# Kernel optimization log

Measured on AMD Instinct MI355X. Metric: run time of the kernel, lower is better.

Reference implementation:

```python
import jax, jax.numpy as jnp
import numpy as np

N_NODES = 50000
N_EDGES = 800000
IN_C = 128
HID_C = 128
OUT_C = 128
ATT_H = 64
EPS_COS = 1e-8
EPS_EUD = 1e-6


def _cos_sim(a, b):
    # torch.cosine_similarity(dim=1): dot / max(|a|*|b|, eps)
    num = jnp.sum(a * b, axis=1)
    den = jnp.maximum(jnp.linalg.norm(a, axis=1) * jnp.linalg.norm(b, axis=1), EPS_COS)
    return num / den


def _eud(a, b):
    # nn.PairwiseDistance(p=2): ||a - b + eps||_2
    d = a - b + EPS_EUD
    return jnp.sqrt(jnp.sum(d * d, axis=1))


def _sage(x, row, col, ew, Wl, bl, Wr):
    # SAGEConv with edge weights: mean_j(ew_ij * x_j) @ Wl + bl + x_i @ Wr
    msg = x[col] * ew[:, None]                               # [E, C]
    agg = jax.ops.segment_sum(msg, row, num_segments=N_NODES)  # [N, C]
    deg = jax.ops.segment_sum(jnp.ones_like(ew), row, num_segments=N_NODES)
    agg = agg / jnp.maximum(deg, 1.0)[:, None]
    return agg @ Wl + bl + x @ Wr


def setup_inputs() -> dict:
    key = jax.random.key(0)
    ks = jax.random.split(key, 12)
    s = 0.05
    return {
        "x": jax.random.normal(ks[0], (N_NODES, IN_C), jnp.float32),
        "row": jax.random.randint(ks[1], (N_EDGES,), 0, N_NODES),
        "col": jax.random.randint(ks[2], (N_EDGES,), 0, N_NODES),
        "Wl0": jax.random.normal(ks[3], (IN_C, HID_C), jnp.float32) * s,
        "bl0": jax.random.normal(ks[4], (HID_C,), jnp.float32) * s,
        "Wr0": jax.random.normal(ks[5], (IN_C, HID_C), jnp.float32) * s,
        "Wl1": jax.random.normal(ks[6], (HID_C, OUT_C), jnp.float32) * s,
        "bl1": jax.random.normal(ks[7], (OUT_C,), jnp.float32) * s,
        "Wr1": jax.random.normal(ks[8], (HID_C, OUT_C), jnp.float32) * s,
        "attW1": jax.random.normal(ks[9], (HID_C, ATT_H), jnp.float32) * s,
        "attb1": jax.random.normal(ks[10], (ATT_H,), jnp.float32) * s,
        "attW2": jax.random.normal(ks[11], (ATT_H, 1), jnp.float32) * s,
    }


def reference(x, row, col, Wl0, bl0, Wr0, Wl1, bl1, Wr1, attW1, attb1, attW2):
    xs, xd = x[row], x[col]
    # cosine branch (dropout is a no-op in eval mode)
    e_cos = _cos_sim(xs, xd)
    x3 = jax.nn.relu(_sage(x, row, col, e_cos, Wl0, bl0, Wr0))   # [N, HID]
    e_cos2 = _cos_sim(x3[row], x3[col])
    x1 = _sage(x3, row, col, e_cos2, Wl1, bl1, Wr1)              # [N, OUT]
    # euclidean branch
    e_eud = _eud(xs, xd)
    x4 = jax.nn.relu(_sage(x, row, col, e_eud, Wl0, bl0, Wr0))   # [N, HID]
    e_eud2 = _eud(x4[row], x4[col])
    x2 = _sage(x4, row, col, e_eud2, Wl1, bl1, Wr1)              # [N, OUT]
    # attention pooling over the 4 branch embeddings
    z = jnp.stack([x1, x2, x3, x4], axis=1)                      # [N, 4, C]
    w = jnp.tanh(z @ attW1 + attb1) @ attW2                      # [N, 4, 1]
    beta = jax.nn.softmax(w, axis=1)
    emb = jnp.sum(beta * z, axis=1)                              # [N, C]
    return (emb, x3, x4)
```

## Files before the change

kernel.cpp:

```cpp
#include <hip/hip_runtime.h>

#define NN 50000
#define NE 800000
#define C 128
#define CAP 64
#define CAPSH 6

typedef __attribute__((ext_vector_type(8))) short short8_t;
typedef __attribute__((ext_vector_type(4))) float f32x4;
typedef __attribute__((ext_vector_type(2))) float f32x2;
typedef __attribute__((ext_vector_type(2))) _Float16 half2_t;
typedef __attribute__((ext_vector_type(8))) _Float16 half8_t;

__device__ __forceinline__ unsigned short f2h_u(float f) {
    _Float16 h = (_Float16)f;
    union { _Float16 h; unsigned short u; } v; v.h = h; return v.u;
}

__device__ __forceinline__ float fdot2(half2_t a, half2_t b, float c) {
#if __has_builtin(__builtin_amdgcn_fdot2)
    return __builtin_amdgcn_fdot2(a, b, c, false);
#else
    return c + (float)a.x * (float)b.x + (float)a.y * (float)b.y;
#endif
}

__device__ __forceinline__ float rsq_fast(float x) {
#if __has_builtin(__builtin_amdgcn_rsqf)
    return __builtin_amdgcn_rsqf(x);
#else
    float r; asm volatile("v_rsq_f32 %0, %1" : "=v"(r) : "v"(x)); return r;
#endif
}
__device__ __forceinline__ float sqrt_fast(float x) {
#if __has_builtin(__builtin_amdgcn_sqrtf)
    return __builtin_amdgcn_sqrtf(x);
#else
    float r; asm volatile("v_sqrt_f32 %0, %1" : "=v"(r) : "v"(x)); return r;
#endif
}

template <int CTRL>
__device__ __forceinline__ float dpp_add(float x) {
    int y = __builtin_amdgcn_update_dpp(0, __float_as_int(x), CTRL, 0xF, 0xF, false);
    return x + __int_as_float(y);
}
__device__ __forceinline__ float qred16(float x) {
    x = dpp_add<0xB1>(x);
    x = dpp_add<0x4E>(x);
    x = dpp_add<0x141>(x);
    x = dpp_add<0x140>(x);
    return x;
}

#define BUCK_NB ((NE / 4 + 255) / 256)
#define CAST_NB (NN / 4)
#define PREP_NB ((65536 + 8192) / 256)
__global__ void cast_prep(const float* __restrict__ x, unsigned short* __restrict__ xh,
                          float2* __restrict__ st1,
                          const float* __restrict__ Wl0, const float* __restrict__ Wr0,
                          const float* __restrict__ Wl1, const float* __restrict__ Wr1,
                          const float* __restrict__ aW1,
                          unsigned short* __restrict__ Bt, unsigned short* __restrict__ BtA,
                          const int* __restrict__ row, const int* __restrict__ col,
                          int* __restrict__ cnt, int* __restrict__ colv) {
    if (blockIdx.x < BUCK_NB) {
        int base = (blockIdx.x * 256 + threadIdx.x) * 4;
        if (base < NE) {
            int4 r4 = *(const int4*)(row + base);
            int4 c4 = *(const int4*)(col + base);
            int p0 = atomicAdd(&cnt[r4.x], 1);
            int p1 = atomicAdd(&cnt[r4.y], 1);
            int p2 = atomicAdd(&cnt[r4.z], 1);
            int p3 = atomicAdd(&cnt[r4.w], 1);
            if (p0 < CAP) colv[(r4.x << CAPSH) + p0] = c4.x;
            if (p1 < CAP) colv[(r4.y << CAPSH) + p1] = c4.y;
            if (p2 < CAP) colv[(r4.z << CAPSH) + p2] = c4.z;
            if (p3 < CAP) colv[(r4.w << CAPSH) + p3] = c4.w;
        }
    } else if (blockIdx.x < BUCK_NB + CAST_NB) {
        int node = (blockIdx.x - BUCK_NB) * 4 + (threadIdx.x >> 6);
        int lane = threadIdx.x & 63;
        float2 v = *(const float2*)(x + (size_t)node * C + lane * 2);
        half2_t h; h.x = (_Float16)v.x; h.y = (_Float16)v.y;
        *(half2_t*)(xh + (size_t)node * C + lane * 2) = h;
        float sq = v.x * v.x + v.y * v.y;
        float sm = v.x + v.y;
#pragma unroll
        for (int off = 32; off > 0; off >>= 1) {
            sq += __shfl_xor(sq, off, 64);
            sm += __shfl_xor(sm, off, 64);
        }
        if (lane == 0) st1[node] = make_float2(sq, sm);
    } else {
        int id = (blockIdx.x - BUCK_NB - CAST_NB) * 256 + threadIdx.x;
        if (id < 65536) {
            int layer = id >> 15;
            int c = (id >> 14) & 1;
            int n = (id >> 7) & 127;
            int kk = id & 127;
            const float* W = layer == 0 ? (c == 0 ? Wl0 : Wr0) : (c == 0 ? Wl1 : Wr1);
            Bt[id] = f2h_u(W[kk * 128 + n]);
        } else {
            int a = id - 65536;
            int cl = a >> 7, k = a & 127;
            BtA[a] = f2h_u(aW1[k * 64 + cl]);
        }
    }
}

__global__ __launch_bounds__(256) void fused_l1(
    const unsigned short* __restrict__ xh, const int* __restrict__ colv,
    const int* __restrict__ cnts, const float2* __restrict__ st1,
    unsigned short* __restrict__ aggc, unsigned short* __restrict__ agge) {
    int node = blockIdx.x * 4 + (threadIdx.x >> 6);
    int lane = threadIdx.x & 63;
    int q = lane >> 4, lq = lane & 15;
    int cnt_raw = cnts[node];
    int cnt = cnt_raw < CAP ? cnt_raw : CAP;
    int cv = colv[(node << CAPSH) + lane];
    half8_t xr = *(const half8_t*)(xh + (size_t)node * C + lq * 8);
    float2 sr = st1[node];
    float n2r = sr.x, s1r = sr.y;
    f32x2 ac[4] = {};
    f32x2 ae[4] = {};
    for (int p = 0; p < cnt; p += 4) {
        int ei = p + q;
        bool valid = ei < cnt;
        int src = valid ? ei : (cnt - 1);
        int c0 = __shfl(cv, src, 64);
        half8_t u = *(const half8_t*)(xh + (size_t)c0 * C + lq * 8);
        float2 t0 = st1[c0];
        float d = 0.f;
#pragma unroll
        for (int i = 0; i < 4; ++i) {
            half2_t a; a.x = xr[2 * i]; a.y = xr[2 * i + 1];
            half2_t b; b.x = u[2 * i]; b.y = u[2 * i + 1];
            d = fdot2(a, b, d);
        }
        d = qred16(d);
        float wc0 = d * rsq_fast(fmaxf(n2r * t0.x, 1e-16f));
        float qq = n2r + t0.x - 2.f * d + 2e-6f * (s1r - t0.y) + 1.28e-10f;
        float we0 = sqrt_fast(fmaxf(qq, 0.f));
        if (!valid) { wc0 = 0.f; we0 = 0.f; }
        f32x2 wcv; wcv.x = wc0; wcv.y = wc0;
        f32x2 wev; wev.x = we0; wev.y = we0;
#pragma unroll
        for (int i = 0; i < 4; ++i) {
            f32x2 uf; uf.x = (float)u[2 * i]; uf.y = (float)u[2 * i + 1];
            ac[i] += wcv * uf;
            ae[i] += wev * uf;
        }
    }
#pragma unroll
    for (int i = 0; i < 4; ++i) {
#pragma unroll
        for (int k = 0; k < 2; ++k) {
            float vc = ac[i][k], ve = ae[i][k];
            vc += __shfl_xor(vc, 16, 64);
            vc += __shfl_xor(vc, 32, 64);
            ve += __shfl_xor(ve, 16, 64);
            ve += __shfl_xor(ve, 32, 64);
            ac[i][k] = vc; ae[i][k] = ve;
        }
    }
    if (q == 0) {
        float inv = 1.f / fmaxf((float)cnt_raw, 1.f);
        half8_t hc, he;
#pragma unroll
        for (int i = 0; i < 4; ++i) {
            hc[2 * i]     = (_Float16)(ac[i].x * inv);
            hc[2 * i + 1] = (_Float16)(ac[i].y * inv);
            he[2 * i]     = (_Float16)(ae[i].x * inv);
            he[2 * i + 1] = (_Float16)(ae[i].y * inv);
        }
        *(half8_t*)(aggc + (size_t)node * C + lq * 8) = hc;
        *(half8_t*)(agge + (size_t)node * C + lq * 8) = he;
    }
}

__global__ __launch_bounds__(256) void fused_l2(
    const unsigned short* __restrict__ x34h,
    const int* __restrict__ colv, const int* __restrict__ cnts,
    const float4* __restrict__ st2,
    unsigned short* __restrict__ agg1, unsigned short* __restrict__ agg2) {
    int node = blockIdx.x * 4 + (threadIdx.x >> 6);
    int lane = threadIdx.x & 63;
    int q = lane >> 4, lq = lane & 15;
    int cnt_raw = cnts[node];
    int cnt = cnt_raw < CAP ? cnt_raw : CAP;
    int cv = colv[(node << CAPSH) + lane];
    const unsigned short* nb = x34h + (size_t)node * 256 + lq * 8;
    half8_t x3r = *(const half8_t*)(nb);
    half8_t x4r = *(const half8_t*)(nb + 128);
    float4 sr = st2[node];
    f32x2 a1[4] = {};
    f32x2 a2[4] = {};
    for (int p = 0; p < cnt; p += 4) {
        int ei = p + q;
        bool valid = ei < cnt;
        int src = valid ? ei : (cnt - 1);
        int c0 = __shfl(cv, src, 64);
        const unsigned short* cb = x34h + (size_t)c0 * 256 + lq * 8;
        half8_t u = *(const half8_t*)(cb);
        half8_t v = *(const half8_t*)(cb + 128);
        float4 t0 = st2[c0];
        float d3 = 0.f, d4 = 0.f;
#pragma unroll
        for (int i = 0; i < 4; ++i) {
            half2_t a; a.x = x3r[2 * i]; a.y = x3r[2 * i + 1];
            half2_t b; b.x = u[2 * i]; b.y = u[2 * i + 1];
            d3 = fdot2(a, b, d3);
            half2_t e; e.x = x4r[2 * i]; e.y = x4r[2 * i + 1];
            half2_t f; f.x = v[2 * i]; f.y = v[2 * i + 1];
            d4 = fdot2(e, f, d4);
        }
        d3 = qred16(d3);
        d4 = qred16(d4);
        float wc0 = d3 * rsq_fast(fmaxf(sr.x * t0.x, 1e-16f));
        float qq = sr.y + t0.y - 2.f * d4 + 2e-6f * (sr.z - t0.z) + 1.28e-10f;
        float we0 = sqrt_fast(fmaxf(qq, 0.f));
        if (!valid) { wc0 = 0.f; we0 = 0.f; }
        f32x2 wcv; wcv.x = wc0; wcv.y = wc0;
        f32x2 wev; wev.x = we0; wev.y = we0;
#pragma unroll
        for (int i = 0; i < 4; ++i) {
            f32x2 uf; uf.x = (float)u[2 * i]; uf.y = (float)u[2 * i + 1];
            f32x2 vf; vf.x = (float)v[2 * i]; vf.y = (float)v[2 * i + 1];
            a1[i] += wcv * uf;
            a2[i] += wev * vf;
        }
    }
#pragma unroll
    for (int i = 0; i < 4; ++i) {
#pragma unroll
        for (int k = 0; k < 2; ++k) {
            float v1 = a1[i][k], v2 = a2[i][k];
            v1 += __shfl_xor(v1, 16, 64);
            v1 += __shfl_xor(v1, 32, 64);
            v2 += __shfl_xor(v2, 16, 64);
            v2 += __shfl_xor(v2, 32, 64);
            a1[i][k] = v1; a2[i][k] = v2;
        }
    }
    if (q == 0) {
        float inv = 1.f / fmaxf((float)cnt_raw, 1.f);
        half8_t h1, h2;
#pragma unroll
        for (int i = 0; i < 4; ++i) {
            h1[2 * i]     = (_Float16)(a1[i].x * inv);
            h1[2 * i + 1] = (_Float16)(a1[i].y * inv);
            h2[2 * i]     = (_Float16)(a2[i].x * inv);
            h2[2 * i + 1] = (_Float16)(a2[i].y * inv);
        }
        *(half8_t*)(agg1 + (size_t)node * C + lq * 8) = h1;
        *(half8_t*)(agg2 + (size_t)node * C + lq * 8) = h2;
    }
}

__global__ __launch_bounds__(256) void gemm_l1(
    const unsigned short* __restrict__ A0a, const unsigned short* __restrict__ A0b,
    const unsigned short* __restrict__ A1,
    const unsigned short* __restrict__ Bt, const float* __restrict__ bias,
    float* __restrict__ Couta, float* __restrict__ Coutb,
    unsigned short* __restrict__ x34h,
    const unsigned short* __restrict__ BtA, const float* __restrict__ ab1,
    const float* __restrict__ aW2,
    float* __restrict__ st2f, float* __restrict__ wout) {
    __shared__ __align__(16) unsigned short sA[128 * 136];
    __shared__ __align__(16) unsigned short sB[128 * 136];
    const int br = blockIdx.y;
    const unsigned short* A0 = br ? A0b : A0a;
    float* Cout = br ? Coutb : Couta;
    unsigned short* Chf = x34h + br * 128;
    const int tx = threadIdx.x;
    const int l = tx & 63;
    const int wv = tx >> 6;
    const int wm = wv >> 1, wn = wv & 1;
    const int lr = l & 15;
    const int lq = l >> 4;
    const int n0 = blockIdx.x * 128;

    f32x4 acc[4][4] = {};
#pragma unroll
    for (int c = 0; c < 2; ++c) {
        const unsigned short* Ac = (c == 0) ? A0 : A1;
#pragma unroll
        for (int it = 0; it < 8; ++it) {
            int idx = it * 256 + tx;
            int r = idx >> 4, s = idx & 15;
            int n = n0 + r; n = n < NN ? n : NN - 1;
            *(short8_t*)(sA + r * 136 + s * 8) = *(const short8_t*)(Ac + (size_t)n * 128 + s * 8);
            *(short8_t*)(sB + r * 136 + s * 8) = *(const short8_t*)(Bt + c * 16384 + idx * 8);
        }
        __syncthreads();
#pragma unroll
        for (int ks = 0; ks < 4; ++ks) {
            half8_t af[4], bfr[4];
#pragma unroll
            for (int t = 0; t < 4; ++t) {
                af[t]  = *(const half8_t*)(sA + (wm * 64 + t * 16 + lr) * 136 + ks * 32 + lq * 8);
                bfr[t] = *(const half8_t*)(sB + (wn * 64 + t * 16 + lr) * 136 + ks * 32 + lq * 8);
            }
#pragma unroll
            for (int mt = 0; mt < 4; ++mt)
#pragma unroll
                for (int nt = 0; nt < 4; ++nt)
                    acc[mt][nt] = __builtin_amdgcn_mfma_f32_16x16x32_f16(af[mt], bfr[nt], acc[mt][nt], 0, 0, 0);
        }
        __syncthreads();
    }
    float* sP2 = (float*)sA;
    float* sP1 = sP2 + 256;
#pragma unroll
    for (int mt = 0; mt < 4; ++mt) {
        int rbase = wm * 64 + mt * 16 + lq * 4;
#pragma unroll
        for (int rg = 0; rg < 4; ++rg) {
            int rloc = rbase + rg;
            int n = n0 + rloc;
            float s2 = 0.f, s1 = 0.f;
#pragma unroll
            for (int nt = 0; nt < 4; ++nt) {
                int col = wn * 64 + nt * 16 + lr;
                float y = acc[mt][nt][rg] + bias[col];
                y = fmaxf(y, 0.f);
                s2 += y * y; s1 += y;
                unsigned short hy = f2h_u(y);
                sB[rloc * 136 + col] = hy;
                if (n < NN) {
                    Cout[(size_t)n * 128 + col] = y;
                    Chf[(size_t)n * 256 + col] = hy;
                }
            }
            s2 = qred16(s2);
            s1 = qred16(s1);
            if (lr == 0) { sP2[rloc * 2 + wn] = s2; sP1[rloc * 2 + wn] = s1; }
        }
    }
    __syncthreads();
    if (tx < 128) {
        int n = n0 + tx;
        if (n < NN) {
            float q2 = sP2[tx * 2] + sP2[tx * 2 + 1];
            if (br == 0) {
                st2f[(size_t)n * 4 + 0] = q2;
            } else {
                st2f[(size_t)n * 4 + 1] = q2;
                st2f[(size_t)n * 4 + 2] = sP1[tx * 2] + sP1[tx * 2 + 1];
            }
        }
    }
    f32x4 sac[2][4] = {};
#pragma unroll
    for (int ks = 0; ks < 4; ++ks) {
        half8_t af[2], bf[4];
#pragma unroll
        for (int mt = 0; mt < 2; ++mt)
            af[mt] = *(const half8_t*)(sB + (wv * 32 + mt * 16 + lr) * 136 + ks * 32 + lq * 8);
#pragma unroll
        for (int nt = 0; nt < 4; ++nt)
            bf[nt] = *(const half8_t*)(BtA + (nt * 16 + lr) * 128 + ks * 32 + lq * 8);
#pragma unroll
        for (int mt = 0; mt < 2; ++mt)
#pragma unroll
            for (int nt = 0; nt < 4; ++nt)
                sac[mt][nt] = __builtin_amdgcn_mfma_f32_16x16x32_f16(af[mt], bf[nt], sac[mt][nt], 0, 0, 0);
    }
#pragma unroll
    for (int mt = 0; mt < 2; ++mt) {
        float part[4] = {0.f, 0.f, 0.f, 0.f};
#pragma unroll
        for (int nt = 0; nt < 4; ++nt) {
            int col = nt * 16 + lr;
            float bb = ab1[col], w2v = aW2[col];
#pragma unroll
            for (int rg = 0; rg < 4; ++rg) {
                float h = sac[mt][nt][rg] + bb;
                float cl = fminf(fmaxf(h, -15.f), 15.f);
                float e2 = __expf(2.f * cl);
                part[rg] += (e2 - 1.f) / (e2 + 1.f) * w2v;
            }
        }
#pragma unroll
        for (int rg = 0; rg < 4; ++rg)
#pragma unroll
            for (int off = 1; off < 16; off <<= 1)
                part[rg] += __shfl_xor(part[rg], off, 64);
        if (lr == 0) {
#pragma unroll
            for (int rg = 0; rg < 4; ++rg) {
                int r = wv * 32 + mt * 16 + lq * 4 + rg;
                int n = n0 + r;
                if (n < NN) wout[(size_t)n * 4 + 2 + br] = part[rg];
            }
        }
    }
}

__global__ __launch_bounds__(256) void gemm2_att(
    const unsigned short* __restrict__ agg1, const unsigned short* __restrict__ agg2,
    const unsigned short* __restrict__ x34h,
    const unsigned short* __restrict__ Bt2, const float* __restrict__ bias,
    const unsigned short* __restrict__ BtA, const float* __restrict__ ab1,
    const float* __restrict__ aW2, const float* __restrict__ wout,
    float* __restrict__ emb) {
    __shared__ __align__(16) unsigned short sA[128 * 136];
    __shared__ __align__(16) unsigned short sB[128 * 136];
    __shared__ float sBeta[128][4];
    const int tx = threadIdx.x;
    const int l = tx & 63;
    const int wv = tx >> 6;
    const int wm = wv >> 1, wn = wv & 1;
    const int lr = l & 15;
    const int lq = l >> 4;
    const int n0 = blockIdx.x * 128;

    f32x4 acc[2][4][4] = {};
#pragma unroll
    for (int br = 0; br < 2; ++br) {
        const unsigned short* A0 = br ? agg2 : agg1;
        const unsigned short* A1 = x34h + br * 128;
#pragma unroll
        for (int c = 0; c < 2; ++c) {
            const unsigned short* Ac = (c == 0) ? A0 : A1;
            const size_t strideA = (c == 0) ? 128 : 256;
#pragma unroll
            for (int it = 0; it < 8; ++it) {
                int idx = it * 256 + tx;
                int r = idx >> 4, s = idx & 15;
                int n = n0 + r; n = n < NN ? n : NN - 1;
                *(short8_t*)(sA + r * 136 + s * 8) = *(const short8_t*)(Ac + (size_t)n * strideA + s * 8);
                *(short8_t*)(sB + r * 136 + s * 8) = *(const short8_t*)(Bt2 + c * 16384 + idx * 8);
            }
            __syncthreads();
#pragma unroll
            for (int ks = 0; ks < 4; ++ks) {
                half8_t af[4], bfr[4];
#pragma unroll
                for (int t = 0; t < 4; ++t) {
                    af[t]  = *(const half8_t*)(sA + (wm * 64 + t * 16 + lr) * 136 + ks * 32 + lq * 8);
                    bfr[t] = *(const half8_t*)(sB + (wn * 64 + t * 16 + lr) * 136 + ks * 32 + lq * 8);
                }
#pragma unroll
                for (int mt = 0; mt < 4; ++mt)
#pragma unroll
                    for (int nt = 0; nt < 4; ++nt)
                        acc[br][mt][nt] = __builtin_amdgcn_mfma_f32_16x16x32_f16(af[mt], bfr[nt], acc[br][mt][nt], 0, 0, 0);
            }
            __syncthreads();
        }
    }
#pragma unroll
    for (int br = 0; br < 2; ++br) {
        unsigned short* sY = br ? sB : sA;
#pragma unroll
        for (int mt = 0; mt < 4; ++mt) {
            int rbase = wm * 64 + mt * 16 + lq * 4;
#pragma unroll
            for (int nt = 0; nt < 4; ++nt) {
                int col = wn * 64 + nt * 16 + lr;
                float bv = bias[col];
#pragma unroll
                for (int rg = 0; rg < 4; ++rg)
                    sY[(rbase + rg) * 136 + col] = f2h_u(acc[br][mt][nt][rg] + bv);
            }
        }
    }
    __syncthreads();
    f32x4 sac[2][2][4] = {};
#pragma unroll
    for (int ks = 0; ks < 4; ++ks) {
        half8_t a1f[2], a2f[2], bf[4];
#pragma unroll
        for (int mt = 0; mt < 2; ++mt) {
            a1f[mt] = *(const half8_t*)(sA + (wv * 32 + mt * 16 + lr) * 136 + ks * 32 + lq * 8);
            a2f[mt] = *(const half8_t*)(sB + (wv * 32 + mt * 16 + lr) * 136 + ks * 32 + lq * 8);
        }
#pragma unroll
        for (int nt = 0; nt < 4; ++nt)
            bf[nt] = *(const half8_t*)(BtA + (nt * 16 + lr) * 128 + ks * 32 + lq * 8);
#pragma unroll
        for (int mt = 0; mt < 2; ++mt)
#pragma unroll
            for (int nt = 0; nt < 4; ++nt) {
                sac[0][mt][nt] = __builtin_amdgcn_mfma_f32_16x16x32_f16(a1f[mt], bf[nt], sac[0][mt][nt], 0, 0, 0);
                sac[1][mt][nt] = __builtin_amdgcn_mfma_f32_16x16x32_f16(a2f[mt], bf[nt], sac[1][mt][nt], 0, 0, 0);
            }
    }
#pragma unroll
    for (int b2 = 0; b2 < 2; ++b2) {
#pragma unroll
        for (int mt = 0; mt < 2; ++mt) {
            float part[4] = {0.f, 0.f, 0.f, 0.f};
#pragma unroll
            for (int nt = 0; nt < 4; ++nt) {
                int col = nt * 16 + lr;
                float bb = ab1[col], w2v = aW2[col];
#pragma unroll
                for (int rg = 0; rg < 4; ++rg) {
                    float h = sac[b2][mt][nt][rg] + bb;
                    float cl = fminf(fmaxf(h, -15.f), 15.f);
                    float e2 = __expf(2.f * cl);
                    part[rg] += (e2 - 1.f) / (e2 + 1.f) * w2v;
                }
            }
#pragma unroll
            for (int rg = 0; rg < 4; ++rg)
#pragma unroll
                for (int off = 1; off < 16; off <<= 1)
                    part[rg] += __shfl_xor(part[rg], off, 64);
            if (lr == 0) {
#pragma unroll
                for (int rg = 0; rg < 4; ++rg) {
                    int r = wv * 32 + mt * 16 + lq * 4 + rg;
                    sBeta[r][b2] = part[rg];
                }
            }
        }
    }
    __syncthreads();
    if (tx < 128) {
        int n = n0 + tx;
        float w1 = sBeta[tx][0], w2v = sBeta[tx][1];
        float w3 = 0.f, w4 = 0.f;
        if (n < NN) {
            w3 = wout[(size_t)n * 4 + 2];
            w4 = wout[(size_t)n * 4 + 3];
        }
        float m = fmaxf(fmaxf(w1, w2v), fmaxf(w3, w4));
        float e1 = __expf(w1 - m), e2 = __expf(w2v - m), e3 = __expf(w3 - m), e4 = __expf(w4 - m);
        float inv = 1.f / (e1 + e2 + e3 + e4);
        sBeta[tx][0] = e1 * inv; sBeta[tx][1] = e2 * inv;
        sBeta[tx][2] = e3 * inv; sBeta[tx][3] = e4 * inv;
    }
    __syncthreads();
#pragma unroll
    for (int pass = 0; pass < 8; ++pass) {
        int r = pass * 16 + (tx >> 4);
        int c0 = (tx & 15) * 8;
        int n = n0 + r;
        if (n < NN) {
            float b1 = sBeta[r][0], b2 = sBeta[r][1], b3 = sBeta[r][2], b4 = sBeta[r][3];
            half8_t y1 = *(const half8_t*)(sA + r * 136 + c0);
            half8_t y2 = *(const half8_t*)(sB + r * 136 + c0);
            half8_t z3 = *(const half8_t*)(x34h + (size_t)n * 256 + c0);
            half8_t z4 = *(const half8_t*)(x34h + (size_t)n * 256 + 128 + c0);
            float o[8];
#pragma unroll
            for (int i = 0; i < 8; ++i)
                o[i] = b1 * (float)y1[i] + b2 * (float)y2[i] + b3 * (float)z3[i] + b4 * (float)z4[i];
            float4 v0; v0.x = o[0]; v0.y = o[1]; v0.z = o[2]; v0.w = o[3];
            float4 v1; v1.x = o[4]; v1.y = o[5]; v1.z = o[6]; v1.w = o[7];
            *(float4*)(emb + (size_t)n * 128 + c0) = v0;
            *(float4*)(emb + (size_t)n * 128 + c0 + 4) = v1;
        }
    }
}

extern "C" void kernel_launch(void* const* d_in, const int* in_sizes, int n_in,
                              void* d_out, int out_size, void* d_ws, size_t ws_size,
                              hipStream_t stream) {
    const float* x   = (const float*)d_in[0];
    const int* row   = (const int*)d_in[1];
    const int* col   = (const int*)d_in[2];
    const float* Wl0 = (const float*)d_in[3];
    const float* bl0 = (const float*)d_in[4];
    const float* Wr0 = (const float*)d_in[5];
    const float* Wl1 = (const float*)d_in[6];
    const float* bl1 = (const float*)d_in[7];
    const float* Wr1 = (const float*)d_in[8];
    const float* aW1 = (const float*)d_in[9];
    const float* ab1 = (const float*)d_in[10];
    const float* aW2 = (const float*)d_in[11];

    float* out = (float*)d_out;
    float* emb = out;
    float* x3  = out + (size_t)NN * C;
    float* x4  = out + 2 * (size_t)NN * C;

    char* ws = (char*)d_ws;
    size_t off = 0;
    auto alloc = [&](size_t bytes) -> void* {
        void* p = ws + off;
        off += (bytes + 255) & ~(size_t)255;
        return p;
    };
    int* cnt     = (int*)alloc((size_t)NN * 4);
    int* colv    = (int*)alloc((size_t)NN * CAP * 4);
    float2* st1  = (float2*)alloc((size_t)NN * 8);
    float4* st2  = (float4*)alloc((size_t)NN * 16);
    unsigned short* xh    = (unsigned short*)alloc((size_t)NN * C * 2);
    unsigned short* aggch = (unsigned short*)alloc((size_t)NN * C * 2);
    unsigned short* aggeh = (unsigned short*)alloc((size_t)NN * C * 2);
    unsigned short* x34h  = (unsigned short*)alloc((size_t)NN * 256 * 2);
    unsigned short* Bt    = (unsigned short*)alloc((size_t)65536 * 2);
    unsigned short* BtA   = (unsigned short*)alloc((size_t)8192 * 2);
    float* wout  = (float*)alloc((size_t)NN * 4 * 4);

    hipMemsetAsync(cnt, 0, (size_t)NN * 4, stream);

    cast_prep<<<BUCK_NB + CAST_NB + PREP_NB, 256, 0, stream>>>(
        x, xh, st1, Wl0, Wr0, Wl1, Wr1, aW1, Bt, BtA, row, col, cnt, colv);

    fused_l1<<<NN / 4, 256, 0, stream>>>(xh, colv, cnt, st1, aggch, aggeh);

    const int GB = (NN + 127) / 128;
    gemm_l1<<<dim3(GB, 2), 256, 0, stream>>>(
        aggch, aggeh, xh, Bt, bl0, x3, x4, x34h,
        BtA, ab1, aW2, (float*)st2, wout);

    fused_l2<<<NN / 4, 256, 0, stream>>>(x34h, colv, cnt, st2, aggch, aggeh);

    gemm2_att<<<GB, 256, 0, stream>>>(
        aggch, aggeh, x34h, Bt + 32768, bl1,
        BtA, ab1, aW2, wout, emb);
}
```

Measured before the change: 363.1 us.

## Split layer-2 GEMM per branch across grid and add separate attention combine kernel

The fused layer-2 GEMM plus attention kernel, which handled both branches serially per 128-row block, becomes a grid of (blocks × 2 branches). Each block computes one branch's GEMM and its attention score and writes the half-precision output to a new x12 buffer. A separate elementwise kernel then does the softmax over the four scores and the weighted combine. This doubles the block count for better occupancy and shortens each block's serial chain, at the cost of an extra kernel launch and an fp16 round trip of x1/x2 through global memory.

Measured after the change: 347.4 us. 1.05x faster.

```diff
diff --git a/kernel.cpp b/kernel.cpp
--- a/kernel.cpp
+++ b/kernel.cpp
@@ -398,16 +398,19 @@
     }
 }
 
-__global__ __launch_bounds__(256) void gemm2_att(
+__global__ __launch_bounds__(256) void gemm_l2(
     const unsigned short* __restrict__ agg1, const unsigned short* __restrict__ agg2,
     const unsigned short* __restrict__ x34h,
     const unsigned short* __restrict__ Bt2, const float* __restrict__ bias,
+    unsigned short* __restrict__ x12h,
     const unsigned short* __restrict__ BtA, const float* __restrict__ ab1,
-    const float* __restrict__ aW2, const float* __restrict__ wout,
-    float* __restrict__ emb) {
+    const float* __restrict__ aW2, float* __restrict__ wout) {
     __shared__ __align__(16) unsigned short sA[128 * 136];
     __shared__ __align__(16) unsigned short sB[128 * 136];
-    __shared__ float sBeta[128][4];
+    const int br = blockIdx.y;
+    const unsigned short* A0 = br ? agg2 : agg1;
+    const unsigned short* A1 = x34h + br * 128;
+    unsigned short* Chf = x12h + br * 128;
     const int tx = threadIdx.x;
     const int l = tx & 63;
     const int wv = tx >> 6;
@@ -416,145 +419,128 @@
     const int lq = l >> 4;
     const int n0 = blockIdx.x * 128;
 
-    f32x4 acc[2][4][4] = {};
-#pragma unroll
-    for (int br = 0; br < 2; ++br) {
-        const unsigned short* A0 = br ? agg2 : agg1;
-        const unsigned short* A1 = x34h + br * 128;
-#pragma unroll
-        for (int c = 0; c < 2; ++c) {
-            const unsigned short* Ac = (c == 0) ? A0 : A1;
-            const size_t strideA = (c == 0) ? 128 : 256;
-#pragma unroll
-            for (int it = 0; it < 8; ++it) {
-                int idx = it * 256 + tx;
-                int r = idx >> 4, s = idx & 15;
-                int n = n0 + r; n = n < NN ? n : NN - 1;
-                *(short8_t*)(sA + r * 136 + s * 8) = *(const short8_t*)(Ac + (size_t)n * strideA + s * 8);
-                *(short8_t*)(sB + r * 136 + s * 8) = *(const short8_t*)(Bt2 + c * 16384 + idx * 8);
-            }
-            __syncthreads();
-#pragma unroll
-            for (int ks = 0; ks < 4; ++ks) {
-                half8_t af[4], bfr[4];
-#pragma unroll
-                for (int t = 0; t < 4; ++t) {
-                    af[t]  = *(const half8_t*)(sA + (wm * 64 + t * 16 + lr) * 136 + ks * 32 + lq * 8);
-                    bfr[t] = *(const half8_t*)(sB + (wn * 64 + t * 16 + lr) * 136 + ks * 32 + lq * 8);
-                }
-#pragma unroll
-                for (int mt = 0; mt < 4; ++mt)
-#pragma unroll
-                    for (int nt = 0; nt < 4; ++nt)
-                        acc[br][mt][nt] = __builtin_amdgcn_mfma_f32_16x16x32_f16(af[mt], bfr[nt], acc[br][mt][nt], 0, 0, 0);
-            }
-            __syncthreads();
-        }
-    }
-#pragma unroll
-    for (int br = 0; br < 2; ++br) {
-        unsigned short* sY = br ? sB : sA;
-#pragma unroll
-        for (int mt = 0; mt < 4; ++mt) {
-            int rbase = wm * 64 + mt * 16 + lq * 4;
+    f32x4 acc[4][4] = {};
+#pragma unroll
+    for (int c = 0; c < 2; ++c) {
+        const unsigned short* Ac = (c == 0) ? A0 : A1;
+        const size_t strideA = (c == 0) ? 128 : 256;
+#pragma unroll
+        for (int it = 0; it < 8; ++it) {
+            int idx = it * 256 + tx;
+            int r = idx >> 4, s = idx & 15;
+            int n = n0 + r; n = n < NN ? n : NN - 1;
+            *(short8_t*)(sA + r * 136 + s * 8) = *(const short8_t*)(Ac + (size_t)n * strideA + s * 8);
+            *(short8_t*)(sB + r * 136 + s * 8) = *(const short8_t*)(Bt2 + c * 16384 + idx * 8);
+        }
+        __syncthreads();
+#pragma unroll
+        for (int ks = 0; ks < 4; ++ks) {
+            half8_t af[4], bfr[4];
+#pragma unroll
+            for (int t = 0; t < 4; ++t) {
+                af[t]  = *(const half8_t*)(sA + (wm * 64 + t * 16 + lr) * 136 + ks * 32 + lq * 8);
+                bfr[t] = *(const half8_t*)(sB + (wn * 64 + t * 16 + lr) * 136 + ks * 32 + lq * 8);
+            }
+#pragma unroll
+            for (int mt = 0; mt < 4; ++mt)
+#pragma unroll
+                for (int nt = 0; nt < 4; ++nt)
+                    acc[mt][nt] = __builtin_amdgcn_mfma_f32_16x16x32_f16(af[mt], bfr[nt], acc[mt][nt], 0, 0, 0);
+        }
+        __syncthreads();
+    }
+#pragma unroll
+    for (int mt = 0; mt < 4; ++mt) {
+        int rbase = wm * 64 + mt * 16 + lq * 4;
+#pragma unroll
+        for (int rg = 0; rg < 4; ++rg) {
+            int rloc = rbase + rg;
+            int n = n0 + rloc;
 #pragma unroll
             for (int nt = 0; nt < 4; ++nt) {
                 int col = wn * 64 + nt * 16 + lr;
-                float bv = bias[col];
-#pragma unroll
-                for (int rg = 0; rg < 4; ++rg)
-                    sY[(rbase + rg) * 136 + col] = f2h_u(acc[br][mt][nt][rg] + bv);
+                float y = acc[mt][nt][rg] + bias[col];
+                unsigned short hy = f2h_u(y);
+                sB[rloc * 136 + col] = hy;
+                if (n < NN) Chf[(size_t)n * 256 + col] = hy;
             }
         }
     }
     __syncthreads();
-    f32x4 sac[2][2][4] = {};
+    f32x4 sac[2][4] = {};
 #pragma unroll
     for (int ks = 0; ks < 4; ++ks) {
-        half8_t a1f[2], a2f[2], bf[4];
-#pragma unroll
-        for (int mt = 0; mt < 2; ++mt) {
-            a1f[mt] = *(const half8_t*)(sA + (wv * 32 + mt * 16 + lr) * 136 + ks * 32 + lq * 8);
-            a2f[mt] = *(const half8_t*)(sB + (wv * 32 + mt * 16 + lr) * 136 + ks * 32 + lq * 8);
-        }
+        half8_t af[2], bf[4];
+#pragma unroll
+        for (int mt = 0; mt < 2; ++mt)
+            af[mt] = *(const half8_t*)(sB + (wv * 32 + mt * 16 + lr) * 136 + ks * 32 + lq * 8);
 #pragma unroll
         for (int nt = 0; nt < 4; ++nt)
             bf[nt] = *(const half8_t*)(BtA + (nt * 16 + lr) * 128 + ks * 32 + lq * 8);
 #pragma unroll
         for (int mt = 0; mt < 2; ++mt)
 #pragma unroll
-            for (int nt = 0; nt < 4; ++nt) {
-                sac[0][mt][nt] = __builtin_amdgcn_mfma_f32_16x16x32_f16(a1f[mt], bf[nt], sac[0][mt][nt], 0, 0, 0);
-                sac[1][mt][nt] = __builtin_amdgcn_mfma_f32_16x16x32_f16(a2f[mt], bf[nt], sac[1][mt][nt], 0, 0, 0);
-            }
-    }
-#pragma unroll
-    for (int b2 = 0; b2 < 2; ++b2) {
-#pragma unroll
-        for (int mt = 0; mt < 2; ++mt) {
-            float part[4] = {0.f, 0.f, 0.f, 0.f};
-#pragma unroll
-            for (int nt = 0; nt < 4; ++nt) {
-                int col = nt * 16 + lr;
-                float bb = ab1[col], w2v = aW2[col];
-#pragma unroll
-                for (int rg = 0; rg < 4; ++rg) {
-                    float h = sac[b2][mt][nt][rg] + bb;
-                    float cl = fminf(fmaxf(h, -15.f), 15.f);
-                    float e2 = __expf(2.f * cl);
-                    part[rg] += (e2 - 1.f) / (e2 + 1.f) * w2v;
-                }
-            }
-#pragma unroll
-            for (int rg = 0; rg < 4; ++rg)
-#pragma unroll
-                for (int off = 1; off < 16; off <<= 1)
-                    part[rg] += __shfl_xor(part[rg], off, 64);
-            if (lr == 0) {
-#pragma unroll
-                for (int rg = 0; rg < 4; ++rg) {
-                    int r = wv * 32 + mt * 16 + lq * 4 + rg;
-                    sBeta[r][b2] = part[rg];
-                }
-            }
-        }
-    }
-    __syncthreads();
-    if (tx < 128) {
-        int n = n0 + tx;
-        float w1 = sBeta[tx][0], w2v = sBeta[tx][1];
-        float w3 = 0.f, w4 = 0.f;
-        if (n < NN) {
-            w3 = wout[(size_t)n * 4 + 2];
-            w4 = wout[(size_t)n * 4 + 3];
-        }
-        float m = fmaxf(fmaxf(w1, w2v), fmaxf(w3, w4));
-        float e1 = __expf(w1 - m), e2 = __expf(w2v - m), e3 = __expf(w3 - m), e4 = __expf(w4 - m);
+            for (int nt = 0; nt < 4; ++nt)
+                sac[mt][nt] = __builtin_amdgcn_mfma_f32_16x16x32_f16(af[mt], bf[nt], sac[mt][nt], 0, 0, 0);
+    }
+#pragma unroll
+    for (int mt = 0; mt < 2; ++mt) {
+        float part[4] = {0.f, 0.f, 0.f, 0.f};
+#pragma unroll
+        for (int nt = 0; nt < 4; ++nt) {
+            int col = nt * 16 + lr;
+            float bb = ab1[col], w2v = aW2[col];
+#pragma unroll
+            for (int rg = 0; rg < 4; ++rg) {
+                float h = sac[mt][nt][rg] + bb;
+                float cl = fminf(fmaxf(h, -15.f), 15.f);
+                float e2 = __expf(2.f * cl);
+                part[rg] += (e2 - 1.f) / (e2 + 1.f) * w2v;
+            }
+        }
+#pragma unroll
+        for (int rg = 0; rg < 4; ++rg)
+#pragma unroll
+            for (int off = 1; off < 16; off <<= 1)
+                part[rg] += __shfl_xor(part[rg], off, 64);
+        if (lr == 0) {
+#pragma unroll
+            for (int rg = 0; rg < 4; ++rg) {
+                int r = wv * 32 + mt * 16 + lq * 4 + rg;
+                int n = n0 + r;
+                if (n < NN) wout[(size_t)n * 4 + br] = part[rg];
+            }
+        }
+    }
+}
+
+__global__ __launch_bounds__(256) void att_combine(
+    const unsigned short* __restrict__ x12h, const unsigned short* __restrict__ x34h,
+    const float* __restrict__ wout, float* __restrict__ emb) {
+    int t = blockIdx.x * 256 + threadIdx.x;
+    int node = t >> 4;
+    int c0 = (t & 15) * 8;
+    if (node < NN) {
+        float4 w = *(const float4*)(wout + (size_t)node * 4);
+        float m = fmaxf(fmaxf(w.x, w.y), fmaxf(w.z, w.w));
+        float e1 = __expf(w.x - m), e2 = __expf(w.y - m), e3 = __expf(w.z - m), e4 = __expf(w.w - m);
         float inv = 1.f / (e1 + e2 + e3 + e4);
-        sBeta[tx][0] = e1 * inv; sBeta[tx][1] = e2 * inv;
-        sBeta[tx][2] = e3 * inv; sBeta[tx][3] = e4 * inv;
-    }
-    __syncthreads();
-#pragma unroll
-    for (int pass = 0; pass < 8; ++pass) {
-        int r = pass * 16 + (tx >> 4);
-        int c0 = (tx & 15) * 8;
-        int n = n0 + r;
-        if (n < NN) {
-            float b1 = sBeta[r][0], b2 = sBeta[r][1], b3 = sBeta[r][2], b4 = sBeta[r][3];
-            half8_t y1 = *(const half8_t*)(sA + r * 136 + c0);
-            half8_t y2 = *(const half8_t*)(sB + r * 136 + c0);
-            half8_t z3 = *(const half8_t*)(x34h + (size_t)n * 256 + c0);
-            half8_t z4 = *(const half8_t*)(x34h + (size_t)n * 256 + 128 + c0);
-            float o[8];
-#pragma unroll
-            for (int i = 0; i < 8; ++i)
-                o[i] = b1 * (float)y1[i] + b2 * (float)y2[i] + b3 * (float)z3[i] + b4 * (float)z4[i];
-            float4 v0; v0.x = o[0]; v0.y = o[1]; v0.z = o[2]; v0.w = o[3];
-            float4 v1; v1.x = o[4]; v1.y = o[5]; v1.z = o[6]; v1.w = o[7];
-            *(float4*)(emb + (size_t)n * 128 + c0) = v0;
-            *(float4*)(emb + (size_t)n * 128 + c0 + 4) = v1;
-        }
+        float b1 = e1 * inv, b2 = e2 * inv, b3 = e3 * inv, b4 = e4 * inv;
+        const unsigned short* p12 = x12h + (size_t)node * 256 + c0;
+        const unsigned short* p34 = x34h + (size_t)node * 256 + c0;
+        half8_t y1 = *(const half8_t*)(p12);
+        half8_t y2 = *(const half8_t*)(p12 + 128);
+        half8_t z3 = *(const half8_t*)(p34);
+        half8_t z4 = *(const half8_t*)(p34 + 128);
+        float o[8];
+#pragma unroll
+        for (int i = 0; i < 8; ++i)
+            o[i] = b1 * (float)y1[i] + b2 * (float)y2[i] + b3 * (float)z3[i] + b4 * (float)z4[i];
+        float4 v0; v0.x = o[0]; v0.y = o[1]; v0.z = o[2]; v0.w = o[3];
+        float4 v1; v1.x = o[4]; v1.y = o[5]; v1.z = o[6]; v1.w = o[7];
+        float* dst = emb + (size_t)node * 128 + c0;
+        *(float4*)(dst) = v0;
+        *(float4*)(dst + 4) = v1;
     }
 }
 
@@ -594,6 +580,7 @@
     unsigned short* aggch = (unsigned short*)alloc((size_t)NN * C * 2);
     unsigned short* aggeh = (unsigned short*)alloc((size_t)NN * C * 2);
     unsigned short* x34h  = (unsigned short*)alloc((size_t)NN * 256 * 2);
+    unsigned short* x12h  = (unsigned short*)alloc((size_t)NN * 256 * 2);
     unsigned short* Bt    = (unsigned short*)alloc((size_t)65536 * 2);
     unsigned short* BtA   = (unsigned short*)alloc((size_t)8192 * 2);
     float* wout  = (float*)alloc((size_t)NN * 4 * 4);
@@ -612,7 +599,9 @@
 
     fused_l2<<<NN / 4, 256, 0, stream>>>(x34h, colv, cnt, st2, aggch, aggeh);
 
-    gemm2_att<<<GB, 256, 0, stream>>>(
+    gemm_l2<<<dim3(GB, 2), 256, 0, stream>>>(
         aggch, aggeh, x34h, Bt + 32768, bl1,
-        BtA, ab1, aW2, wout, emb);
-}
+        x12h, BtA, ab1, aW2, wout);
+
+    att_combine<<<(NN * 16 + 255) / 256, 256, 0, stream>>>(x12h, x34h, wout, emb);
+}
```
